# Optimization experiments

Hardware: AMD Instinct MI355X
Metric: run time of the kernel (lower is better)

Reference implementation:

```python
import jax, jax.numpy as jnp
import numpy as np

B, T, C, H, N = 4, 4096, 1024, 16, 64
D_DECAY, D_AAA, D_MV, D_GATE = 64, 64, 32, 160
EPS_GN = 1e-5 * 8 ** 2  # GroupNorm eps = 1e-5 * head_size_divisor**2


def _k(i):
    return jax.random.fold_in(jax.random.key(0), i)


def setup_inputs():
    p = {}
    p["x"] = jax.random.normal(_k(1), (B, T, C), jnp.float32)
    p["v_first"] = jax.random.normal(_k(2), (B, T, C), jnp.float32)
    for i, name in enumerate(["x_r", "x_w", "x_k", "x_v", "x_a", "x_g"]):
        p[name] = jax.random.uniform(_k(10 + i), (1, 1, C), jnp.float32)
    p["w0"] = jnp.linspace(-7.0, -2.0, C, dtype=jnp.float32).reshape(1, 1, C) + 0.5
    p["w1"] = jax.random.normal(_k(20), (C, D_DECAY), jnp.float32) * 0.02
    p["w2"] = jax.random.normal(_k(21), (D_DECAY, C), jnp.float32) * 0.02
    p["a0"] = jax.random.normal(_k(22), (1, 1, C), jnp.float32) * 0.02
    p["a1"] = jax.random.normal(_k(23), (C, D_AAA), jnp.float32) * 0.02
    p["a2"] = jax.random.normal(_k(24), (D_AAA, C), jnp.float32) * 0.02
    p["v0"] = jnp.ones((1, 1, C), jnp.float32)
    p["v1"] = jax.random.normal(_k(25), (C, D_MV), jnp.float32) * 0.02
    p["v2"] = jax.random.normal(_k(26), (D_MV, C), jnp.float32) * 0.02
    p["g1"] = jax.random.normal(_k(27), (C, D_GATE), jnp.float32) * 0.02
    p["g2"] = jax.random.normal(_k(28), (D_GATE, C), jnp.float32) * 0.02
    p["k_k"] = jnp.full((1, 1, C), 0.85, jnp.float32)
    p["k_a"] = jnp.ones((1, 1, C), jnp.float32)
    p["r_k"] = jax.random.normal(_k(29), (H, N), jnp.float32) * 0.02
    s = 0.5 / C ** 0.5
    p["Wr"] = jax.random.uniform(_k(30), (C, C), jnp.float32, -s, s)
    p["Wk"] = jax.random.uniform(_k(31), (C, C), jnp.float32, -0.1 * s, 0.1 * s)
    p["Wv"] = jax.random.uniform(_k(32), (C, C), jnp.float32, -s, s)
    p["Wo"] = jax.random.uniform(_k(33), (C, C), jnp.float32, -s, s)
    p["ln_w"] = jnp.ones((C,), jnp.float32)
    p["ln_b"] = jnp.zeros((C,), jnp.float32)
    p["alpha"] = jnp.array(0.5, jnp.float32)
    return p


def _wkv_scan(ins, reverse):
    # ins: tuple of time-major (T,B,H,N) arrays: r, decay, k, v, a, b
    def step(S, inp):
        r_t, d_t, k_t, v_t, a_t, b_t = inp
        sa = jnp.einsum('bhij,bhj->bhi', S, a_t)  # in-context removal term
        S = (S * d_t[:, :, None, :]
             + sa[..., None] * b_t[:, :, None, :]
             + v_t[..., None] * k_t[:, :, None, :])
        return S, jnp.einsum('bhij,bhj->bhi', S, r_t)
    S0 = jnp.zeros((B, H, N, N), jnp.float32)
    return jax.lax.scan(step, S0, ins, reverse=reverse)[1]


def reference(x, v_first, x_r, x_w, x_k, x_v, x_a, x_g, w0, w1, w2, a0, a1, a2,
              v0, v1, v2, g1, g2, k_k, k_a, r_k, Wr, Wk, Wv, Wo, ln_w, ln_b, alpha):
    xx = jnp.pad(x, ((0, 0), (1, 0), (0, 0)))[:, :T, :] - x  # token shift
    xr = x + xx * x_r
    xw = x + xx * x_w
    xk = x + xx * x_k
    xv = x + xx * x_v
    xa = x + xx * x_a
    xg = x + xx * x_g
    r = xr @ Wr.T
    w = -jax.nn.softplus(-(w0 + jnp.tanh(xw @ w1) @ w2)) - 0.5
    k = xk @ Wk.T
    v = xv @ Wv.T
    v = v + (v_first - v) * jax.nn.sigmoid(v0 + (xv @ v1) @ v2)  # layer_id != 0
    a = jax.nn.sigmoid(a0 + (xa @ a1) @ a2)
    g = jax.nn.sigmoid(xg @ g1) @ g2
    kk = (k * k_k).reshape(B, T, H, N)
    kk = kk / jnp.maximum(jnp.linalg.norm(kk, axis=-1, keepdims=True), 1e-12)
    k = k * (1.0 + (a - 1.0) * k_a)
    rh = r.reshape(B, T, H, N)
    kh = k.reshape(B, T, H, N)
    vh = v.reshape(B, T, H, N)
    dec = jnp.exp(-jnp.exp(w.reshape(B, T, H, N)))  # per-channel decay
    ah = -kk
    bh = kk * a.reshape(B, T, H, N)
    tm = lambda z: jnp.transpose(z, (1, 0, 2, 3))  # -> (T,B,H,N)
    ins = (tm(rh), tm(dec), tm(kh), tm(vh), tm(ah), tm(bh))
    y_f = _wkv_scan(ins, reverse=False)
    y_b = _wkv_scan(ins, reverse=True)
    y = alpha * y_f + (1.0 - alpha) * y_b  # bidirectional blend (alpha)
    y = jnp.transpose(y, (1, 0, 2, 3))  # (B,T,H,N)
    mu = y.mean(-1, keepdims=True)
    var = y.var(-1, keepdims=True)
    y = (y - mu) / jnp.sqrt(var + EPS_GN)  # GroupNorm(H groups)
    y = y * ln_w.reshape(1, 1, H, N) + ln_b.reshape(1, 1, H, N)
    y = y + (rh * kh * r_k).sum(-1, keepdims=True) * vh
    out = (y.reshape(B, T, C) * g) @ Wo.T
    return (out, v_first)
```

## Files before the change

### kernel.cpp

```cpp
#include <hip/hip_runtime.h>
#include <hip/hip_bf16.h>
#include <math.h>

#define BB 4
#define TT 4096
#define CC 1024
#define HH 16
#define NN 64
#define BT (BB*TT)
#define EPS_GN 6.4e-4f
#define TMAX (TT-1)
#define LCH 64
#define CB 8
#define NB 8
#define STR 68

typedef __attribute__((ext_vector_type(8))) short bf16x8;
typedef __attribute__((ext_vector_type(4))) float f32x4;

__device__ __forceinline__ float sigmoidf_(float x) {
    return 1.0f / (1.0f + expf(-x));
}

__device__ __forceinline__ float waveReduceSum(float v) {
    #pragma unroll
    for (int off = 32; off > 0; off >>= 1)
        v += __shfl_xor(v, off, 64);
    return v;
}

__device__ __forceinline__ unsigned short f2bf(float f) {
    unsigned u = __float_as_uint(f);
    u += 0x7FFFu + ((u >> 16) & 1u);
    return (unsigned short)(u >> 16);
}
__device__ __forceinline__ float bf2f(unsigned short h) {
    return __uint_as_float(((unsigned)h) << 16);
}

__device__ __forceinline__ void gll16(const unsigned short* g, unsigned short* l) {
    __builtin_amdgcn_global_load_lds(
        (__attribute__((address_space(1))) void*)(g),
        (__attribute__((address_space(3))) void*)(l), 16, 0, 0);
}

template<int SA0,int SA1,int SB0,int SB1>
__device__ __forceinline__ void gemm64(const float* __restrict__ A,
                                       const float* __restrict__ B,
                                       float acc[4][4], int tr, int tc) {
    #pragma unroll 2
    for (int kx = 0; kx < 64; kx += 4) {
        float a_[4][4];
        if (SA0 == 1) {
            #pragma unroll
            for (int kk = 0; kk < 4; kk++) {
                float4 t = *(const float4*)&A[tr + (kx + kk) * SA1];
                a_[0][kk] = t.x; a_[1][kk] = t.y; a_[2][kk] = t.z; a_[3][kk] = t.w;
            }
        } else {
            #pragma unroll
            for (int r = 0; r < 4; r++) {
                float4 t = *(const float4*)&A[(tr + r) * SA0 + kx];
                a_[r][0] = t.x; a_[r][1] = t.y; a_[r][2] = t.z; a_[r][3] = t.w;
            }
        }
        float b_[4][4];
        if (SB0 == 1) {
            #pragma unroll
            for (int kk = 0; kk < 4; kk++) {
                float4 t = *(const float4*)&B[tc + (kx + kk) * SB1];
                b_[0][kk] = t.x; b_[1][kk] = t.y; b_[2][kk] = t.z; b_[3][kk] = t.w;
            }
        } else {
            #pragma unroll
            for (int cq = 0; cq < 4; cq++) {
                float4 t = *(const float4*)&B[(tc + cq) * SB0 + kx];
                b_[cq][0] = t.x; b_[cq][1] = t.y; b_[cq][2] = t.z; b_[cq][3] = t.w;
            }
        }
        #pragma unroll
        for (int r = 0; r < 4; r++)
            #pragma unroll
            for (int cq = 0; cq < 4; cq++)
                #pragma unroll
                for (int kk = 0; kk < 4; kk++)
                    acc[r][cq] = fmaf(a_[r][kk], b_[cq][kk], acc[r][cq]);
    }
}

template<bool DOMIX>
__global__ __launch_bounds__(256) void conv_split(
    const float* __restrict__ X, const float* __restrict__ mix,
    unsigned short* __restrict__ Hi, unsigned short* __restrict__ Lo,
    int ngroups)
{
    int g = blockIdx.x * 256 + threadIdx.x;
    if (g >= ngroups) return;
    int m = g >> 7;
    int k = (g & 127) * 8;
    const float* px = X + (size_t)m * CC + k;
    float a[8];
    {
        float4 x0 = *(const float4*)px;
        float4 x1 = *(const float4*)(px + 4);
        a[0]=x0.x; a[1]=x0.y; a[2]=x0.z; a[3]=x0.w;
        a[4]=x1.x; a[5]=x1.y; a[6]=x1.z; a[7]=x1.w;
    }
    if (DOMIX) {
        float4 p0, p1;
        if ((m & (TT - 1)) == 0) {
            p0 = make_float4(0.f,0.f,0.f,0.f); p1 = p0;
        } else {
            p0 = *(const float4*)(px - CC);
            p1 = *(const float4*)(px - CC + 4);
        }
        float4 m0 = *(const float4*)(mix + k);
        float4 m1 = *(const float4*)(mix + k + 4);
        float pv[8] = {p0.x,p0.y,p0.z,p0.w,p1.x,p1.y,p1.z,p1.w};
        float mv[8] = {m0.x,m0.y,m0.z,m0.w,m1.x,m1.y,m1.z,m1.w};
        #pragma unroll
        for (int j = 0; j < 8; j++) a[j] += (pv[j] - a[j]) * mv[j];
    }
    unsigned short hi[8], lo[8];
    #pragma unroll
    for (int j = 0; j < 8; j++) {
        hi[j] = f2bf(a[j]);
        lo[j] = f2bf(a[j] - bf2f(hi[j]));
    }
    uint4 H, L;
    H.x = (unsigned)hi[0] | ((unsigned)hi[1] << 16);
    H.y = (unsigned)hi[2] | ((unsigned)hi[3] << 16);
    H.z = (unsigned)hi[4] | ((unsigned)hi[5] << 16);
    H.w = (unsigned)hi[6] | ((unsigned)hi[7] << 16);
    L.x = (unsigned)lo[0] | ((unsigned)lo[1] << 16);
    L.y = (unsigned)lo[2] | ((unsigned)lo[3] << 16);
    L.z = (unsigned)lo[4] | ((unsigned)lo[5] << 16);
    L.w = (unsigned)lo[6] | ((unsigned)lo[7] << 16);
    *(uint4*)(Hi + (size_t)g * 8) = H;
    *(uint4*)(Lo + (size_t)g * 8) = L;
}

__global__ __launch_bounds__(256) void conv_w2(
    const float* __restrict__ W, int K, int Kp,
    unsigned short* __restrict__ Hi, unsigned short* __restrict__ Lo)
{
    int idx = blockIdx.x * 256 + threadIdx.x;
    int nk8 = Kp >> 3;
    if (idx >= CC * nk8) return;
    int n = idx / nk8, k0 = (idx - n * nk8) * 8;
    unsigned short h8[8], l8[8];
    #pragma unroll
    for (int j = 0; j < 8; j++) {
        int k = k0 + j;
        float v = (k < K) ? W[(size_t)k * CC + n] : 0.f;
        h8[j] = f2bf(v);
        l8[j] = f2bf(v - bf2f(h8[j]));
    }
    uint4 H, L;
    H.x = (unsigned)h8[0] | ((unsigned)h8[1] << 16);
    H.y = (unsigned)h8[2] | ((unsigned)h8[3] << 16);
    H.z = (unsigned)h8[4] | ((unsigned)h8[5] << 16);
    H.w = (unsigned)h8[6] | ((unsigned)h8[7] << 16);
    L.x = (unsigned)l8[0] | ((unsigned)l8[1] << 16);
    L.y = (unsigned)l8[2] | ((unsigned)l8[3] << 16);
    L.z = (unsigned)l8[4] | ((unsigned)l8[5] << 16);
    L.w = (unsigned)l8[6] | ((unsigned)l8[7] << 16);
    *(uint4*)(Hi + (size_t)n * Kp + k0) = H;
    *(uint4*)(Lo + (size_t)n * Kp + k0) = L;
}

__global__ __launch_bounds__(256, 2) void gemm_split_bf16(
    const unsigned short* __restrict__ Ah, const unsigned short* __restrict__ Al,
    const unsigned short* __restrict__ Bh, const unsigned short* __restrict__ Bl,
    float* __restrict__ Out)
{
    __shared__ __align__(16) unsigned short lds[4][128 * 64];
    const int tid = threadIdx.x;
    const int lane = tid & 63;
    const int wave = tid >> 6;
    const int wm = (wave >> 1) * 64, wn = (wave & 1) * 64;
    const int wg = blockIdx.x;
    const int xcd = wg & 7;
    const int j = wg >> 3;
    const int m0 = ((j >> 3) * 8 + xcd) * 128;
    const int n0 = (j & 7) * 128;

    f32x4 acc[4][4];
    #pragma unroll
    for (int i = 0; i < 4; i++)
        #pragma unroll
        for (int jj = 0; jj < 4; jj++)
            acc[i][jj] = (f32x4){0.f, 0.f, 0.f, 0.f};

    for (int k0 = 0; k0 < CC; k0 += 64) {
        #pragma unroll
        for (int p = 0; p < 4; p++) {
            const unsigned short* sbase = (p == 0) ? Ah : (p == 1) ? Al
                                        : (p == 2) ? Bh : Bl;
            const int rbase = (p < 2) ? m0 : n0;
            #pragma unroll
            for (int i = 0; i < 4; i++) {
                int slot = i * 256 + wave * 64 + lane;
                int row = slot >> 3, gsl = slot & 7;
                const unsigned short* src = sbase
                    + (size_t)(rbase + row) * CC + k0 + ((gsl ^ (row & 7)) * 8);
                gll16(src, &lds[p][(size_t)(i * 256 + wave * 64) * 8]);
            }
        }
        __syncthreads();

        #pragma unroll
        for (int ks = 0; ks < 2; ks++) {
            bf16x8 bhf[4], blf[4];
            #pragma unroll
            for (int nt = 0; nt < 4; nt++) {
                int col = wn + nt * 16 + (lane & 15);
                int gk = ks * 4 + (lane >> 4);
                int el = col * 64 + ((gk ^ (col & 7)) * 8);
                bhf[nt] = *(const bf16x8*)&lds[2][el];
                blf[nt] = *(const bf16x8*)&lds[3][el];
            }
            #pragma unroll
            for (int mt = 0; mt < 4; mt++) {
                int row = wm + mt * 16 + (lane & 15);
                int gk = ks * 4 + (lane >> 4);
                int el = row * 64 + ((gk ^ (row & 7)) * 8);
                bf16x8 ahf = *(const bf16x8*)&lds[0][el];
                bf16x8 alf = *(const bf16x8*)&lds[1][el];
                #pragma unroll
                for (int nt = 0; nt < 4; nt++) {
                    acc[mt][nt] = __builtin_amdgcn_mfma_f32_16x16x32_bf16(
                        ahf, bhf[nt], acc[mt][nt], 0, 0, 0);
                    acc[mt][nt] = __builtin_amdgcn_mfma_f32_16x16x32_bf16(
                        alf, bhf[nt], acc[mt][nt], 0, 0, 0);
                    acc[mt][nt] = __builtin_amdgcn_mfma_f32_16x16x32_bf16(
                        ahf, blf[nt], acc[mt][nt], 0, 0, 0);
                }
            }
        }
        __syncthreads();
    }
    float* cf = (float*)&lds[0][0];
    #pragma unroll
    for (int pass = 0; pass < 2; ++pass) {
        __syncthreads();
        if ((wave >> 1) == pass) {
            #pragma unroll
            for (int mt = 0; mt < 4; mt++)
                #pragma unroll
                for (int nt = 0; nt < 4; nt++)
                    #pragma unroll
                    for (int r = 0; r < 4; r++) {
                        int row = mt * 16 + (lane >> 4) * 4 + r;
                        int col = wn + nt * 16 + (lane & 15);
                        cf[row * 132 + col] = acc[mt][nt][r];
                    }
        }
        __syncthreads();
        #pragma unroll
        for (int i = 0; i < 8; i++) {
            int g = tid + 256 * i;
            int row = g >> 5, c4 = (g & 31) * 4;
            float4 v = *(float4*)&cf[row * 132 + c4];
            *(float4*)&Out[(size_t)(m0 + pass * 64 + row) * CC + n0 + c4] = v;
        }
    }
}

__global__ __launch_bounds__(256) void lora1_all(
    const float* __restrict__ X,
    const float* __restrict__ w1, const float* __restrict__ a1,
    const float* __restrict__ v1, const float* __restrict__ g1,
    const float* __restrict__ xw, const float* __restrict__ xa,
    const float* __restrict__ xv, const float* __restrict__ xg,
    unsigned short* __restrict__ awh, unsigned short* __restrict__ awl,
    unsigned short* __restrict__ aah, unsigned short* __restrict__ aal,
    unsigned short* __restrict__ avh, unsigned short* __restrict__ avl,
    unsigned short* __restrict__ agh, unsigned short* __restrict__ agl)
{
    const int y = blockIdx.y;
    const float* W; const float* mix; unsigned short *Hi, *Lo;
    int Ncols, n0, epi, Kp;
    if (y == 0)      { W=w1; mix=xw; Hi=awh; Lo=awl; Ncols=64;  n0=0;          epi=1; Kp=64;  }
    else if (y == 1) { W=a1; mix=xa; Hi=aah; Lo=aal; Ncols=64;  n0=0;          epi=0; Kp=64;  }
    else if (y == 2) { W=v1; mix=xv; Hi=avh; Lo=avl; Ncols=32;  n0=0;          epi=0; Kp=64;  }
    else             { W=g1; mix=xg; Hi=agh; Lo=agl; Ncols=160; n0=(y-3)*64;   epi=2; Kp=192; }

    __shared__ float As[8][128];
    __shared__ float Bs[8][64];
    const int tid = threadIdx.x;
    const int m0 = blockIdx.x * 128;
    const int sr  = tid >> 1;
    const int skq = (tid & 1) * 4;
    const int bkr = tid >> 4;
    const int bnq = (tid & 15) * 4;
    const int tm = (tid >> 3) * 4;
    const int tn = (tid & 7) * 8;

    float acc[4][8];
    #pragma unroll
    for (int i = 0; i < 4; i++)
        #pragma unroll
        for (int j = 0; j < 8; j++) acc[i][j] = 0.f;

    auto ldAm = [&](int gm, int gk) -> float4 {
        const float* px = X + (size_t)gm * CC + gk;
        float4 xvv = *(const float4*)px;
        float4 pv;
        if ((gm & (TT - 1)) == 0) pv = make_float4(0.f, 0.f, 0.f, 0.f);
        else pv = *(const float4*)(px - CC);
        float4 mv = *(const float4*)(mix + gk);
        xvv.x += (pv.x - xvv.x) * mv.x;
        xvv.y += (pv.y - xvv.y) * mv.y;
        xvv.z += (pv.z - xvv.z) * mv.z;
        xvv.w += (pv.w - xvv.w) * mv.w;
        return xvv;
    };

    float4 aR, bR = make_float4(0.f, 0.f, 0.f, 0.f);
    aR = ldAm(m0 + sr, skq);
    if (tid < 128) {
        int gn = n0 + bnq;
        bR = (gn < Ncols) ? *(const float4*)(W + (size_t)bkr * Ncols + gn)
                          : make_float4(0.f, 0.f, 0.f, 0.f);
    }

    for (int k0 = 0; k0 < CC; k0 += 8) {
        __syncthreads();
        As[skq + 0][sr] = aR.x;
        As[skq + 1][sr] = aR.y;
        As[skq + 2][sr] = aR.z;
        As[skq + 3][sr] = aR.w;
        if (tid < 128) *(float4*)&Bs[bkr][bnq] = bR;
        __syncthreads();

        if (k0 + 8 < CC) {
            aR = ldAm(m0 + sr, k0 + 8 + skq);
            if (tid < 128) {
                int gn = n0 + bnq;
                bR = (gn < Ncols) ? *(const float4*)(W + (size_t)(k0 + 8 + bkr) * Ncols + gn)
                                  : make_float4(0.f, 0.f, 0.f, 0.f);
            }
        }

        #pragma unroll
        for (int kk = 0; kk < 8; ++kk) {
            float av[4], bv[8];
            *(float4*)&av[0] = *(const float4*)&As[kk][tm];
            *(float4*)&bv[0] = *(const float4*)&Bs[kk][tn];
            *(float4*)&bv[4] = *(const float4*)&Bs[kk][tn + 4];
            #pragma unroll
            for (int i = 0; i < 4; i++)
                #pragma unroll
                for (int j = 0; j < 8; j++)
                    acc[i][j] = fmaf(av[i], bv[j], acc[i][j]);
        }
    }

    #pragma unroll
    for (int i = 0; i < 4; i++) {
        int gm = m0 + tm + i;
        int gn = n0 + tn;
        if (gn < Kp) {
            unsigned short h8[8], l8[8];
            #pragma unroll
            for (int j = 0; j < 8; j++) {
                float v = 0.f;
                if (gn + j < Ncols) {
                    v = acc[i][j];
                    if (epi == 1) v = tanhf(v);
                    else if (epi == 2) v = sigmoidf_(v);
                }
                h8[j] = f2bf(v);
                l8[j] = f2bf(v - bf2f(h8[j]));
            }
            uint4 H, L;
            H.x = (unsigned)h8[0] | ((unsigned)h8[1] << 16);
            H.y = (unsigned)h8[2] | ((unsigned)h8[3] << 16);
            H.z = (unsigned)h8[4] | ((unsigned)h8[5] << 16);
            H.w = (unsigned)h8[6] | ((unsigned)h8[7] << 16);
            L.x = (unsigned)l8[0] | ((unsigned)l8[1] << 16);
            L.y = (unsigned)l8[2] | ((unsigned)l8[3] << 16);
            L.z = (unsigned)l8[4] | ((unsigned)l8[5] << 16);
            L.w = (unsigned)l8[6] | ((unsigned)l8[7] << 16);
            *(uint4*)(Hi + (size_t)gm * Kp + gn) = H;
            *(uint4*)(Lo + (size_t)gm * Kp + gn) = L;
        }
    }
}

__global__ __launch_bounds__(256, 2) void lora2_mfma(
    const unsigned short* __restrict__ awh, const unsigned short* __restrict__ awl,
    const unsigned short* __restrict__ aah, const unsigned short* __restrict__ aal,
    const unsigned short* __restrict__ avh, const unsigned short* __restrict__ avl,
    const unsigned short* __restrict__ agh, const unsigned short* __restrict__ agl,
    const unsigned short* __restrict__ w2h, const unsigned short* __restrict__ w2l,
    const unsigned short* __restrict__ a2h, const unsigned short* __restrict__ a2l,
    const unsigned short* __restrict__ v2h, const unsigned short* __restrict__ v2l,
    const unsigned short* __restrict__ g2h, const unsigned short* __restrict__ g2l,
    const float* __restrict__ w0, const float* __restrict__ a0v,
    const float* __restrict__ v0v, const float* __restrict__ v_first,
    float* __restrict__ decb, float* __restrict__ ab,
    float* __restrict__ vbuf, float* __restrict__ gb)
{
    __shared__ __align__(16) unsigned short lds[4][128 * 64];
    const int z = blockIdx.z;
    const unsigned short *Ah, *Al, *Bh, *Bl; int Kp;
    if (z == 0)      { Ah = awh; Al = awl; Bh = w2h; Bl = w2l; Kp = 64;  }
    else if (z == 1) { Ah = aah; Al = aal; Bh = a2h; Bl = a2l; Kp = 64;  }
    else if (z == 2) { Ah = avh; Al = avl; Bh = v2h; Bl = v2l; Kp = 64;  }
    else             { Ah = agh; Al = agl; Bh = g2h; Bl = g2l; Kp = 192; }

    const int tid = threadIdx.x, lane = tid & 63, wave = tid >> 6;
    const int wm = (wave >> 1) * 64, wn = (wave & 1) * 64;
    const int m0 = blockIdx.x * 128, n0 = blockIdx.y * 128;

    f32x4 acc[4][4];
    #pragma unroll
    for (int i = 0; i < 4; i++)
        #pragma unroll
        for (int jj = 0; jj < 4; jj++)
            acc[i][jj] = (f32x4){0.f, 0.f, 0.f, 0.f};

    for (int k0 = 0; k0 < Kp; k0 += 64) {
        #pragma unroll
        for (int p = 0; p < 4; p++) {
            const unsigned short* sbase = (p == 0) ? Ah : (p == 1) ? Al
                                        : (p == 2) ? Bh : Bl;
            const int rbase = (p < 2) ? m0 : n0;
            #pragma unroll
            for (int i = 0; i < 4; i++) {
                int slot = i * 256 + wave * 64 + lane;
                int row = slot >> 3, gsl = slot & 7;
                const unsigned short* src = sbase
                    + (size_t)(rbase + row) * Kp + k0 + ((gsl ^ (row & 7)) * 8);
                gll16(src, &lds[p][(size_t)(i * 256 + wave * 64) * 8]);
            }
        }
        __syncthreads();

        #pragma unroll
        for (int ks = 0; ks < 2; ks++) {
            bf16x8 bhf[4], blf[4];
            #pragma unroll
            for (int nt = 0; nt < 4; nt++) {
                int col = wn + nt * 16 + (lane & 15);
                int gk = ks * 4 + (lane >> 4);
                int el = col * 64 + ((gk ^ (col & 7)) * 8);
                bhf[nt] = *(const bf16x8*)&lds[2][el];
                blf[nt] = *(const bf16x8*)&lds[3][el];
            }
            #pragma unroll
            for (int mt = 0; mt < 4; mt++) {
                int row = wm + mt * 16 + (lane & 15);
                int gk = ks * 4 + (lane >> 4);
                int el = row * 64 + ((gk ^ (row & 7)) * 8);
                bf16x8 ahf = *(const bf16x8*)&lds[0][el];
                bf16x8 alf = *(const bf16x8*)&lds[1][el];
                #pragma unroll
                for (int nt = 0; nt < 4; nt++) {
                    acc[mt][nt] = __builtin_amdgcn_mfma_f32_16x16x32_bf16(
                        ahf, bhf[nt], acc[mt][nt], 0, 0, 0);
                    acc[mt][nt] = __builtin_amdgcn_mfma_f32_16x16x32_bf16(
                        alf, bhf[nt], acc[mt][nt], 0, 0, 0);
                    acc[mt][nt] = __builtin_amdgcn_mfma_f32_16x16x32_bf16(
                        ahf, blf[nt], acc[mt][nt], 0, 0, 0);
                }
            }
        }
        __syncthreads();
    }
    float* cf = (float*)&lds[0][0];
    #pragma unroll
    for (int pass = 0; pass < 2; ++pass) {
        __syncthreads();
        if ((wave >> 1) == pass) {
            #pragma unroll
            for (int mt = 0; mt < 4; mt++)
                #pragma unroll
                for (int nt = 0; nt < 4; nt++)
                    #pragma unroll
                    for (int r = 0; r < 4; r++) {
                        int row = mt * 16 + (lane >> 4) * 4 + r;
                        int col = wn + nt * 16 + (lane & 15);
                        cf[row * 132 + col] = acc[mt][nt][r];
                    }
        }
        __syncthreads();
        #pragma unroll
        for (int i = 0; i < 8; i++) {
            int g = tid + 256 * i;
            int row = g >> 5, c4 = (g & 31) * 4;
            float4 v = *(float4*)&cf[row * 132 + c4];
            int gm = m0 + pass * 64 + row;
            int c = n0 + c4;
            size_t off = (size_t)gm * CC + c;
            if (z == 0) {
                float4 w0q = *(const float4*)(w0 + c);
                float4 o;
                o.x = expf(-expf(-log1pf(expf(-(w0q.x + v.x))) - 0.5f));
                o.y = expf(-expf(-log1pf(expf(-(w0q.y + v.y))) - 0.5f));
                o.z = expf(-expf(-log1pf(expf(-(w0q.z + v.z))) - 0.5f));
                o.w = expf(-expf(-log1pf(expf(-(w0q.w + v.w))) - 0.5f));
                *(float4*)&decb[off] = o;
            } else if (z == 1) {
                float4 a0q = *(const float4*)(a0v + c);
                float4 o;
                o.x = sigmoidf_(a0q.x + v.x);
                o.y = sigmoidf_(a0q.y + v.y);
                o.z = sigmoidf_(a0q.z + v.z);
                o.w = sigmoidf_(a0q.w + v.w);
                *(float4*)&ab[off] = o;
            } else if (z == 2) {
                float4 v0q = *(const float4*)(v0v + c);
                float4 vr = *(const float4*)&vbuf[off];
                float4 vf = *(const float4*)&v_first[off];
                float4 o;
                o.x = vr.x + (vf.x - vr.x) * sigmoidf_(v0q.x + v.x);
                o.y = vr.y + (vf.y - vr.y) * sigmoidf_(v0q.y + v.y);
                o.z = vr.z + (vf.z - vr.z) * sigmoidf_(v0q.z + v.z);
                o.w = vr.w + (vf.w - vr.w) * sigmoidf_(v0q.w + v.w);
                *(float4*)&vbuf[off] = o;
            } else {
                *(float4*)&gb[off] = v;
            }
        }
    }
}

__global__ __launch_bounds__(256) void wkvA(
    const float* __restrict__ kb, const float* __restrict__ ab,
    const float* __restrict__ vb, const float* __restrict__ decb,
    const float* __restrict__ k_k, const float* __restrict__ k_a,
    float* __restrict__ Gb, float* __restrict__ Ub,
    float* __restrict__ Bpb, float* __restrict__ Kpb,
    float* __restrict__ wcb, int cb)
{
    __shared__ __align__(16) float sAp[64 * STR];
    __shared__ __align__(16) float sBp[64 * STR];
    __shared__ __align__(16) float sKp[64 * STR];
    __shared__ __align__(16) float sT [64 * STR];
    __shared__ float sSeg[4][64];
    const int inst = blockIdx.x;
    const int bhd = inst >> 3, lc = inst & 7;
    const int dir = bhd & 1, bh = bhd >> 1, b = bh >> 4, h = bh & 15;
    const int c64 = (cb * CB + lc) * LCH;
    const int tid = threadIdx.x;
    const int lane = tid & 63, seg = tid >> 6;
    const int ch = h * 64 + lane;
    const size_t gbase = (size_t)inst * 4096;

    float loc[16];
    {
        float run = 1.f;
        #pragma unroll
        for (int i = 0; i < 16; i++) {
            int p = seg * 16 + i;
            int t = dir ? (TMAX - (c64 + p)) : (c64 + p);
            float d = decb[((size_t)(b * TT + t)) * CC + ch];
            run *= d; loc[i] = run;
        }
        sSeg[seg][lane] = run;
    }
    __syncthreads();
    float pre = 1.f;
    for (int s2 = 0; s2 < seg; ++s2) pre *= sSeg[s2][lane];
    {
        const float kkl = k_k[ch], kal = k_a[ch];
        #pragma unroll
        for (int i = 0; i < 16; i++) {
            int p = seg * 16 + i;
            int t = dir ? (TMAX - (c64 + p)) : (c64 + p);
            size_t ra = ((size_t)(b * TT + t)) * CC + ch;
            float kraw = kb[ra], asig = ab[ra];
            float kkv = kraw * kkl;
            float s2 = waveReduceSum(kkv * kkv);
            float kkn = kkv / fmaxf(sqrtf(s2), 1e-12f);
            float wc = loc[i] * pre;
            float wx = (i == 0) ? pre : loc[i - 1] * pre;
            float apv = -kkn * wx;
            float bpv = kkn * asig / wc;
            float kpv = kraw * (1.f + (asig - 1.f) * kal) / wc;
            sAp[lane * STR + p] = apv;
            sBp[lane * STR + p] = bpv;
            sKp[lane * STR + p] = kpv;
            Bpb[gbase + p * 64 + lane] = bpv;
            Kpb[gbase + p * 64 + lane] = kpv;
            wcb[gbase + p * 64 + lane] = wc;
        }
    }
    __syncthreads();

    const int tr = (tid >> 4) * 4, tc = (tid & 15) * 4;
    {
        float acc[4][4] = {};
        gemm64<1, STR, 1, STR>(sAp, sKp, acc, tr, tc);
        #pragma unroll
        for (int r = 0; r < 4; r++)
            #pragma unroll
            for (int cq = 0; cq < 4; cq++)
                sT[(tr + r) * STR + tc + cq] = (tc + cq < tr + r) ? acc[r][cq] : 0.f;
    }
    __syncthreads();
    {
        float accY[4][4] = {};
        const float* vbase = vb + ((size_t)(b * TT + (dir ? (TMAX - c64) : c64))) * CC
                           + h * 64 + tc;
        const ptrdiff_t vstep = dir ? -(ptrdiff_t)CC : (ptrdiff_t)CC;
        #pragma unroll 2
        for (int j4 = 0; j4 < 64; j4 += 4) {
            float a_[4][4];
            #pragma unroll
            for (int r = 0; r < 4; r++) {
                float4 t4 = *(const float4*)&sT[(tr + r) * STR + j4];
                a_[r][0] = t4.x; a_[r][1] = t4.y; a_[r][2] = t4.z; a_[r][3] = t4.w;
            }
            float4 vq[4];
            #pragma unroll
            for (int kk = 0; kk < 4; kk++)
                vq[kk] = *(const float4*)(vbase + (ptrdiff_t)(j4 + kk) * vstep);
            #pragma unroll
            for (int r = 0; r < 4; r++) {
                accY[r][0] = fmaf(a_[r][0], vq[0].x, fmaf(a_[r][1], vq[1].x,
                             fmaf(a_[r][2], vq[2].x, fmaf(a_[r][3], vq[3].x, accY[r][0]))));
                accY[r][1] = fmaf(a_[r][0], vq[0].y, fmaf(a_[r][1], vq[1].y,
                             fmaf(a_[r][2], vq[2].y, fmaf(a_[r][3], vq[3].y, accY[r][1]))));
                accY[r][2] = fmaf(a_[r][0], vq[0].z, fmaf(a_[r][1], vq[1].z,
                             fmaf(a_[r][2], vq[2].z, fmaf(a_[r][3], vq[3].z, accY[r][2]))));
                accY[r][3] = fmaf(a_[r][0], vq[0].w, fmaf(a_[r][1], vq[1].w,
                             fmaf(a_[r][2], vq[2].w, fmaf(a_[r][3], vq[3].w, accY[r][3]))));
            }
        }
        #pragma unroll
        for (int r = 0; r < 4; r++)
            #pragma unroll
            for (int cq = 0; cq < 4; cq++)
                sKp[(tr + r) * STR + tc + cq] = accY[r][cq];
    }
    __syncthreads();
    {
        float acc[4][4] = {};
        gemm64<1, STR, 1, STR>(sAp, sBp, acc, tr, tc);
        #pragma unroll
        for (int r = 0; r < 4; r++)
            #pragma unroll
            for (int cq = 0; cq < 4; cq++)
                sT[(tr + r) * STR + tc + cq] = (tc + cq < tr + r) ? acc[r][cq] : 0.f;
    }
    __syncthreads();
    if (tid < 64) {
        for (int r = 0; r < 64; ++r) {
            float acc = 0.f;
            for (int s = 0; s < r; ++s)
                acc = fmaf(sT[r * STR + s], sBp[s * STR + tid], acc);
            sBp[r * STR + tid] = (r == tid) ? 1.f : acc;
        }
    }
    __syncthreads();
    {
        float accG[4][4] = {};
        gemm64<STR, 1, STR, 1>(sBp, sAp, accG, tr, tc);
        float accU[4][4] = {};
        gemm64<STR, 1, 1, STR>(sBp, sKp, accU, tr, tc);
        #pragma unroll
        for (int r = 0; r < 4; r++) {
            *(float4*)&Gb[gbase + (tr + r) * 64 + tc] =
                make_float4(accG[r][0], accG[r][1], accG[r][2], accG[r][3]);
            *(float4*)&Ub[gbase + (tr + r) * 64 + tc] =
                make_float4(accU[r][0], accU[r][1], accU[r][2], accU[r][3]);
        }
    }
}

__global__ __launch_bounds__(256) void wkvB(
    const float* __restrict__ vb,
    const float* __restrict__ Gb, float* __restrict__ Ub,
    const float* __restrict__ Bpb, const float* __restrict__ Kpb,
    const float* __restrict__ wcb, float* __restrict__ S0b,
    float* __restrict__ Scur, int cb)
{
    __shared__ __align__(16) float sS[64 * STR];
    __shared__ __align__(16) float sG[64 * STR];
    __shared__ __align__(16) float sU[64 * STR];
    __shared__ __align__(16) float sB[64 * STR];
    __shared__ __align__(16) float sK[64 * STR];
    __shared__ __align__(16) float sV[64 * STR];
    const int bhd = blockIdx.x;
    const int dir = bhd & 1, bh = bhd >> 1, b = bh >> 4, h = bh & 15;
    const int tid = threadIdx.x;
    const int tr = (tid >> 4) * 4, tc = (tid & 15) * 4;

    for (int i = tid; i < 4096; i += 256)
        sS[(i >> 6) * STR + (i & 63)] = Scur[(size_t)bhd * 4096 + i];
    __syncthreads();

    for (int lc = 0; lc < CB; ++lc) {
        const int inst = bhd * CB + lc;
        const size_t gbase = (size_t)inst * 4096;
        const int c64 = (cb * CB + lc) * LCH;
        for (int i = tid; i < 4096; i += 256) {
            int rr = i >> 6, jj = i & 63;
            sG[rr * STR + jj] = Gb[gbase + i];
            sB[rr * STR + jj] = Bpb[gbase + i];
            sK[rr * STR + jj] = Kpb[gbase + i];
            int t = dir ? (TMAX - (c64 + rr)) : (c64 + rr);
            sV[rr * STR + jj] = vb[((size_t)(b * TT + t)) * CC + h * 64 + jj];
            S0b[gbase + i] = sS[rr * STR + jj];
        }
        __syncthreads();
        {
            float acc[4][4];
            #pragma unroll
            for (int r = 0; r < 4; r++) {
                float4 u0 = *(const float4*)&Ub[gbase + (tr + r) * 64 + tc];
                acc[r][0] = u0.x; acc[r][1] = u0.y; acc[r][2] = u0.z; acc[r][3] = u0.w;
            }
            gemm64<STR, 1, STR, 1>(sG, sS, acc, tr, tc);
            #pragma unroll
            for (int r = 0; r < 4; r++) {
                #pragma unroll
                for (int cq = 0; cq < 4; cq++) sU[(tr + r) * STR + tc + cq] = acc[r][cq];
                *(float4*)&Ub[gbase + (tr + r) * 64 + tc] =
                    make_float4(acc[r][0], acc[r][1], acc[r][2], acc[r][3]);
            }
        }
        __syncthreads();
        {
            float acc[4][4] = {};
            gemm64<1, STR, 1, STR>(sU, sB, acc, tr, tc);
            gemm64<1, STR, 1, STR>(sV, sK, acc, tr, tc);
            float w63[4];
            #pragma unroll
            for (int cq = 0; cq < 4; cq++) w63[cq] = wcb[gbase + 63 * 64 + tc + cq];
            #pragma unroll
            for (int r = 0; r < 4; r++)
                #pragma unroll
                for (int cq = 0; cq < 4; cq++) {
                    float sv = sS[(tr + r) * STR + tc + cq];
                    acc[r][cq] = (sv + acc[r][cq]) * w63[cq];
                }
            #pragma unroll
            for (int r = 0; r < 4; r++)
                #pragma unroll
                for (int cq = 0; cq < 4; cq++)
                    sS[(tr + r) * STR + tc + cq] = acc[r][cq];
        }
        __syncthreads();
    }
    for (int i = tid; i < 4096; i += 256)
        Scur[(size_t)bhd * 4096 + i] = sS[(i >> 6) * STR + (i & 63)];
}

__global__ __launch_bounds__(256) void wkvC(
    const float* __restrict__ rb, const float* __restrict__ vb,
    const float* __restrict__ Bpb, const float* __restrict__ Kpb,
    const float* __restrict__ Ub, const float* __restrict__ S0b,
    const float* __restrict__ wcb, const float* __restrict__ alpha_p,
    float* __restrict__ yb, int cb)
{
    __shared__ __align__(16) float sR[64 * STR];
    __shared__ __align__(16) float sO[64 * STR];
    __shared__ __align__(16) float sT2[64 * STR];
    const int inst = blockIdx.x;
    const int bhd = inst >> 3, lc = inst & 7;
    const int dir = bhd & 1, bh = bhd >> 1, b = bh >> 4, h = bh & 15;
    const int c64 = (cb * CB + lc) * LCH;
    const int tid = threadIdx.x, lane = tid & 63, seg = tid >> 6;
    const size_t gbase = (size_t)inst * 4096;
    const float alpha = alpha_p[0];
    const float wscale = dir ? (1.f - alpha) : alpha;
    const bool first = (cb < NB / 2);

    #pragma unroll
    for (int i = 0; i < 16; i++) {
        int p = seg * 16 + i;
        int t = dir ? (TMAX - (c64 + p)) : (c64 + p);
        size_t ra = ((size_t)(b * TT + t)) * CC + h * 64 + lane;
        float wc = wcb[gbase + p * 64 + lane];
        sR[lane * STR + p] = rb[ra] * wc;
        sO[lane * STR + p] = Bpb[gbase + p * 64 + lane];
    }
    __syncthreads();
    const int tr = (tid >> 4) * 4, tc = (tid & 15) * 4;
    float accO[4][4] = {};
    {
        float acc[4][4] = {};
        gemm64<1, STR, 1, STR>(sR, sO, acc, tr, tc);
        #pragma unroll
        for (int r = 0; r < 4; r++)
            #pragma unroll
            for (int cq = 0; cq < 4; cq++)
                sT2[(tr + r) * STR + tc + cq] = (tc + cq <= tr + r) ? acc[r][cq] : 0.f;
    }
    __syncthreads();
    for (int i = tid; i < 4096; i += 256)
        sO[(i >> 6) * STR + (i & 63)] = Ub[gbase + i];
    __syncthreads();
    gemm64<STR, 1, 1, STR>(sT2, sO, accO, tr, tc);
    __syncthreads();
    #pragma unroll
    for (int i = 0; i < 16; i++) {
        int p = seg * 16 + i;
        sO[lane * STR + p] = Kpb[gbase + p * 64 + lane];
    }
    __syncthreads();
    {
        float acc[4][4] = {};
        gemm64<1, STR, 1, STR>(sR, sO, acc, tr, tc);
        #pragma unroll
        for (int r = 0; r < 4; r++)
            #pragma unroll
            for (int cq = 0; cq < 4; cq++)
                sT2[(tr + r) * STR + tc + cq] = (tc + cq <= tr + r) ? acc[r][cq] : 0.f;
    }
    __syncthreads();
    #pragma unroll
    for (int i = 0; i < 16; i++) {
        int p = seg * 16 + i;
        int t = dir ? (TMAX - (c64 + p)) : (c64 + p);
        sO[p * STR + lane] = vb[((size_t)(b * TT + t)) * CC + h * 64 + lane];
    }
    __syncthreads();
    gemm64<STR, 1, 1, STR>(sT2, sO, accO, tr, tc);
    __syncthreads();
    for (int i = tid; i < 4096; i += 256)
        sO[(i >> 6) * STR + (i & 63)] = S0b[gbase + i];
    __syncthreads();
    gemm64<1, STR, STR, 1>(sR, sO, accO, tr, tc);
    #pragma unroll
    for (int r = 0; r < 4; r++) {
        int p = tr + r;
        int t = dir ? (TMAX - (c64 + p)) : (c64 + p);
        float* yp = &yb[((size_t)(b * TT + t)) * CC + h * 64 + tc];
        float4 o;
        if (first) {
            o.x = wscale * accO[r][0];
            o.y = wscale * accO[r][1];
            o.z = wscale * accO[r][2];
            o.w = wscale * accO[r][3];
        } else {
            float4 old = *(float4*)yp;
            o.x = old.x + wscale * accO[r][0];
            o.y = old.y + wscale * accO[r][1];
            o.z = old.z + wscale * accO[r][2];
            o.w = old.w + wscale * accO[r][3];
        }
        *(float4*)yp = o;
    }
}

__global__ __launch_bounds__(256) void post_kernel(
    const float* __restrict__ yb, const float* __restrict__ rbv,
    const float* __restrict__ kbv, const float* __restrict__ abv,
    const float* __restrict__ vbv, const float* __restrict__ gbv,
    const float* __restrict__ kaw, const float* __restrict__ r_k,
    const float* __restrict__ ln_w, const float* __restrict__ ln_b,
    unsigned short* __restrict__ zh, unsigned short* __restrict__ zl)
{
    const int t = blockIdx.x;
    const int tid = threadIdx.x;
    const size_t base = (size_t)t * CC;
    #pragma unroll
    for (int j = 0; j < 4; j++) {
        int c = tid + 256 * j;
        float y = yb[base + c];
        float s1 = waveReduceSum(y);
        float s2 = waveReduceSum(y * y);
        float mu = s1 * (1.0f / 64.0f);
        float var = s2 * (1.0f / 64.0f) - mu * mu;
        float yn = (y - mu) * rsqrtf(var + EPS_GN);
        yn = yn * ln_w[c] + ln_b[c];
        float rv = rbv[base + c];
        float kf = kbv[base + c] * (1.0f + (abv[base + c] - 1.0f) * kaw[c]);
        float vv = vbv[base + c];
        float dot = waveReduceSum(rv * kf * r_k[c]);
        yn += dot * vv;
        float z = yn * gbv[base + c];
        unsigned short h = f2bf(z);
        zh[base + c] = h;
        zl[base + c] = f2bf(z - bf2f(h));
    }
}

extern "C" void kernel_launch(void* const* d_in, const int* in_sizes, int n_in,
                              void* d_out, int out_size, void* d_ws, size_t ws_size,
                              hipStream_t stream)
{
    (void)in_sizes; (void)n_in; (void)out_size; (void)ws_size;
    const float* x      = (const float*)d_in[0];
    const float* vfirst = (const float*)d_in[1];
    const float* x_r    = (const float*)d_in[2];
    const float* x_w    = (const float*)d_in[3];
    const float* x_k    = (const float*)d_in[4];
    const float* x_v    = (const float*)d_in[5];
    const float* x_a    = (const float*)d_in[6];
    const float* x_g    = (const float*)d_in[7];
    const float* w0     = (const float*)d_in[8];
    const float* w1     = (const float*)d_in[9];
    const float* w2     = (const float*)d_in[10];
    const float* a0     = (const float*)d_in[11];
    const float* a1     = (const float*)d_in[12];
    const float* a2     = (const float*)d_in[13];
    const float* v0     = (const float*)d_in[14];
    const float* v1     = (const float*)d_in[15];
    const float* v2     = (const float*)d_in[16];
    const float* g1     = (const float*)d_in[17];
    const float* g2     = (const float*)d_in[18];
    const float* k_k    = (const float*)d_in[19];
    const float* k_a    = (const float*)d_in[20];
    const float* r_k    = (const float*)d_in[21];
    const float* Wr     = (const float*)d_in[22];
    const float* Wk     = (const float*)d_in[23];
    const float* Wv     = (const float*)d_in[24];
    const float* Wo     = (const float*)d_in[25];
    const float* ln_w   = (const float*)d_in[26];
    const float* ln_b   = (const float*)d_in[27];
    const float* alpha  = (const float*)d_in[28];

    const size_t SZ = (size_t)BT * CC;
    const size_t CHB = (size_t)1024 * 4096;
    float* ws   = (float*)d_ws;
    float* rb   = ws + 0 * SZ;
    float* kb   = ws + 1 * SZ;
    float* vb   = ws + 2 * SZ;
    float* decb = ws + 3 * SZ;
    float* ab   = ws + 4 * SZ;
    float* actf = ws + 5 * SZ;
    unsigned short* awh = (unsigned short*)actf;
    unsigned short* awl = awh + (size_t)BT * 64;
    unsigned short* aah = awl + (size_t)BT * 64;
    unsigned short* aal = aah + (size_t)BT * 64;
    unsigned short* avh = aal + (size_t)BT * 64;
    unsigned short* avl = avh + (size_t)BT * 64;
    unsigned short* agh = avl + (size_t)BT * 64;
    unsigned short* agl = agh + (size_t)BT * 192;
    float* Gb   = actf + (size_t)BT * 384;
    float* Ub   = Gb + CHB;
    float* Bpb  = Ub + CHB;
    float* Kpb  = Bpb + CHB;
    float* S0b  = Kpb + CHB;
    float* wcb  = S0b + CHB;
    float* Scur = wcb + CHB;
    unsigned short* Whb = (unsigned short*)(Scur + (size_t)128 * 4096);
    unsigned short* Wlb = Whb + (size_t)CC * CC;
    unsigned short* w2th = Wlb + (size_t)CC * CC;
    unsigned short* w2tl = w2th + (size_t)CC * 64;
    unsigned short* a2th = w2tl + (size_t)CC * 64;
    unsigned short* a2tl = a2th + (size_t)CC * 64;
    unsigned short* v2th = a2tl + (size_t)CC * 64;
    unsigned short* v2tl = v2th + (size_t)CC * 64;
    unsigned short* g2th = v2tl + (size_t)CC * 64;
    unsigned short* g2tl = g2th + (size_t)CC * 192;
    float* outp = (float*)d_out;
    float* gb   = outp;
    float* yb   = outp + SZ;
    unsigned short* Ahp = (unsigned short*)(outp + SZ);
    unsigned short* Alp = Ahp + SZ;
    unsigned short* zAh = (unsigned short*)decb;
    unsigned short* zAl = zAh + SZ;

    dim3 blk(256);
    const int NG_A = BT * (CC / 8);
    const int NG_W = CC * (CC / 8);
    dim3 gridA(NG_A / 256), gridW(NG_W / 256);
    dim3 gridG(1024);

    conv_split<false><<<gridW, blk, 0, stream>>>(Wr, nullptr, Whb, Wlb, NG_W);
    conv_split<true ><<<gridA, blk, 0, stream>>>(x, x_r, Ahp, Alp, NG_A);
    gemm_split_bf16<<<gridG, blk, 0, stream>>>(Ahp, Alp, Whb, Wlb, rb);
    conv_split<false><<<gridW, blk, 0, stream>>>(Wk, nullptr, Whb, Wlb, NG_W);
    conv_split<true ><<<gridA, blk, 0, stream>>>(x, x_k, Ahp, Alp, NG_A);
    gemm_split_bf16<<<gridG, blk, 0, stream>>>(Ahp, Alp, Whb, Wlb, kb);
    conv_split<false><<<gridW, blk, 0, stream>>>(Wv, nullptr, Whb, Wlb, NG_W);
    conv_split<true ><<<gridA, blk, 0, stream>>>(x, x_v, Ahp, Alp, NG_A);
    gemm_split_bf16<<<gridG, blk, 0, stream>>>(Ahp, Alp, Whb, Wlb, vb);

    conv_w2<<<dim3(32), blk, 0, stream>>>(w2, 64, 64, w2th, w2tl);
    conv_w2<<<dim3(32), blk, 0, stream>>>(a2, 64, 64, a2th, a2tl);
    conv_w2<<<dim3(32), blk, 0, stream>>>(v2, 32, 64, v2th, v2tl);
    conv_w2<<<dim3(96), blk, 0, stream>>>(g2, 160, 192, g2th, g2tl);

    lora1_all<<<dim3(BT / 128, 6), blk, 0, stream>>>(x, w1, a1, v1, g1,
        x_w, x_a, x_v, x_g, awh, awl, aah, aal, avh, avl, agh, agl);
    lora2_mfma<<<dim3(BT / 128, CC / 128, 4), blk, 0, stream>>>(
        awh, awl, aah, aal, avh, avl, agh, agl,
        w2th, w2tl, a2th, a2tl, v2th, v2tl, g2th, g2tl,
        w0, a0, v0, vfirst, decb, ab, vb, gb);

    hipMemsetAsync(Scur, 0, (size_t)128 * 4096 * sizeof(float), stream);
    for (int cb = 0; cb < NB; ++cb) {
        wkvA<<<dim3(1024), blk, 0, stream>>>(kb, ab, vb, decb, k_k, k_a,
                                             Gb, Ub, Bpb, Kpb, wcb, cb);
        wkvB<<<dim3(128), blk, 0, stream>>>(vb, Gb, Ub, Bpb, Kpb, wcb, S0b, Scur, cb);
        wkvC<<<dim3(1024), blk, 0, stream>>>(rb, vb, Bpb, Kpb, Ub, S0b, wcb,
                                             alpha, yb, cb);
    }

    post_kernel<<<dim3(BT), blk, 0, stream>>>(yb, rb, kb, ab, vb, gb, k_a, r_k,
                                              ln_w, ln_b, zAh, zAl);
    conv_split<false><<<gridW, blk, 0, stream>>>(Wo, nullptr, Whb, Wlb, NG_W);
    hipMemcpyAsync(outp + SZ, vfirst, SZ * sizeof(float),
                   hipMemcpyDeviceToDevice, stream);
    gemm_split_bf16<<<gridG, blk, 0, stream>>>(zAh, zAl, Whb, Wlb, outp);
}
```

Measured before the change: 3.212 ms.

## Fuse token-shift bf16 split for r/k/v inputs and retile lora2 to 128x64

A new kernel reads x and its shifted row once and writes the bf16 hi/lo splits for the r, k and v mixes together. This replaces three separate conversion passes that each re-read x. The lora2 MFMA kernel moves from 128x128 to 128x64 tiles with less LDS and a simpler single-pass epilogue, so more blocks fit per CU. In exchange, the r/k/v split buffers now live in the output and decay scratch regions, which must not be overwritten before the GEMMs consume them.

Result: faster. 3.111 ms (-3.1%).

```diff
diff --git a/kernel.cpp b/kernel.cpp
--- a/kernel.cpp
+++ b/kernel.cpp
@@ -138,6 +138,63 @@
     L.w = (unsigned)lo[6] | ((unsigned)lo[7] << 16);
     *(uint4*)(Hi + (size_t)g * 8) = H;
     *(uint4*)(Lo + (size_t)g * 8) = L;
+}
+
+__global__ __launch_bounds__(256) void conv_split_x3(
+    const float* __restrict__ X,
+    const float* __restrict__ mr, const float* __restrict__ mk,
+    const float* __restrict__ mv,
+    unsigned short* __restrict__ rH, unsigned short* __restrict__ rL,
+    unsigned short* __restrict__ kH, unsigned short* __restrict__ kL,
+    unsigned short* __restrict__ vH, unsigned short* __restrict__ vL)
+{
+    int g = blockIdx.x * 256 + threadIdx.x;
+    int m = g >> 7;
+    int k = (g & 127) * 8;
+    const float* px = X + (size_t)m * CC + k;
+    float xv8[8], pv[8];
+    {
+        float4 x0 = *(const float4*)px;
+        float4 x1 = *(const float4*)(px + 4);
+        xv8[0]=x0.x; xv8[1]=x0.y; xv8[2]=x0.z; xv8[3]=x0.w;
+        xv8[4]=x1.x; xv8[5]=x1.y; xv8[6]=x1.z; xv8[7]=x1.w;
+    }
+    if ((m & (TT - 1)) == 0) {
+        #pragma unroll
+        for (int j = 0; j < 8; j++) pv[j] = 0.f;
+    } else {
+        float4 p0 = *(const float4*)(px - CC);
+        float4 p1 = *(const float4*)(px - CC + 4);
+        pv[0]=p0.x; pv[1]=p0.y; pv[2]=p0.z; pv[3]=p0.w;
+        pv[4]=p1.x; pv[5]=p1.y; pv[6]=p1.z; pv[7]=p1.w;
+    }
+    const float* mixes[3] = {mr, mk, mv};
+    unsigned short* His[3] = {rH, kH, vH};
+    unsigned short* Los[3] = {rL, kL, vL};
+    #pragma unroll
+    for (int s = 0; s < 3; s++) {
+        float4 m0 = *(const float4*)(mixes[s] + k);
+        float4 m1 = *(const float4*)(mixes[s] + k + 4);
+        float mv8[8] = {m0.x,m0.y,m0.z,m0.w,m1.x,m1.y,m1.z,m1.w};
+        unsigned short hi[8], lo[8];
+        #pragma unroll
+        for (int j = 0; j < 8; j++) {
+            float a = xv8[j] + (pv[j] - xv8[j]) * mv8[j];
+            hi[j] = f2bf(a);
+            lo[j] = f2bf(a - bf2f(hi[j]));
+        }
+        uint4 H, L;
+        H.x = (unsigned)hi[0] | ((unsigned)hi[1] << 16);
+        H.y = (unsigned)hi[2] | ((unsigned)hi[3] << 16);
+        H.z = (unsigned)hi[4] | ((unsigned)hi[5] << 16);
+        H.w = (unsigned)hi[6] | ((unsigned)hi[7] << 16);
+        L.x = (unsigned)lo[0] | ((unsigned)lo[1] << 16);
+        L.y = (unsigned)lo[2] | ((unsigned)lo[3] << 16);
+        L.z = (unsigned)lo[4] | ((unsigned)lo[5] << 16);
+        L.w = (unsigned)lo[6] | ((unsigned)lo[7] << 16);
+        *(uint4*)(His[s] + (size_t)g * 8) = H;
+        *(uint4*)(Los[s] + (size_t)g * 8) = L;
+    }
 }
 
 __global__ __launch_bounds__(256) void conv_w2(
@@ -389,7 +446,7 @@
     }
 }
 
-__global__ __launch_bounds__(256, 2) void lora2_mfma(
+__global__ __launch_bounds__(256, 3) void lora2_mfma(
     const unsigned short* __restrict__ awh, const unsigned short* __restrict__ awl,
     const unsigned short* __restrict__ aah, const unsigned short* __restrict__ aal,
     const unsigned short* __restrict__ avh, const unsigned short* __restrict__ avl,
@@ -403,7 +460,7 @@
     float* __restrict__ decb, float* __restrict__ ab,
     float* __restrict__ vbuf, float* __restrict__ gb)
 {
-    __shared__ __align__(16) unsigned short lds[4][128 * 64];
+    __shared__ __align__(16) unsigned short lds[24576];
     const int z = blockIdx.z;
     const unsigned short *Ah, *Al, *Bh, *Bl; int Kp;
     if (z == 0)      { Ah = awh; Al = awl; Bh = w2h; Bl = w2l; Kp = 64;  }
@@ -412,53 +469,63 @@
     else             { Ah = agh; Al = agl; Bh = g2h; Bl = g2l; Kp = 192; }
 
     const int tid = threadIdx.x, lane = tid & 63, wave = tid >> 6;
-    const int wm = (wave >> 1) * 64, wn = (wave & 1) * 64;
-    const int m0 = blockIdx.x * 128, n0 = blockIdx.y * 128;
-
-    f32x4 acc[4][4];
+    const int wm = (wave >> 1) * 64, wn = (wave & 1) * 32;
+    const int m0 = blockIdx.x * 128, n0 = blockIdx.y * 64;
+
+    f32x4 acc[4][2];
     #pragma unroll
     for (int i = 0; i < 4; i++)
         #pragma unroll
-        for (int jj = 0; jj < 4; jj++)
+        for (int jj = 0; jj < 2; jj++)
             acc[i][jj] = (f32x4){0.f, 0.f, 0.f, 0.f};
 
     for (int k0 = 0; k0 < Kp; k0 += 64) {
         #pragma unroll
-        for (int p = 0; p < 4; p++) {
-            const unsigned short* sbase = (p == 0) ? Ah : (p == 1) ? Al
-                                        : (p == 2) ? Bh : Bl;
-            const int rbase = (p < 2) ? m0 : n0;
+        for (int p = 0; p < 2; p++) {
+            const unsigned short* sbase = (p == 0) ? Ah : Al;
             #pragma unroll
             for (int i = 0; i < 4; i++) {
                 int slot = i * 256 + wave * 64 + lane;
                 int row = slot >> 3, gsl = slot & 7;
                 const unsigned short* src = sbase
-                    + (size_t)(rbase + row) * Kp + k0 + ((gsl ^ (row & 7)) * 8);
-                gll16(src, &lds[p][(size_t)(i * 256 + wave * 64) * 8]);
+                    + (size_t)(m0 + row) * Kp + k0 + ((gsl ^ (row & 7)) * 8);
+                gll16(src, &lds[(size_t)(p * 8192) + (size_t)(i * 256 + wave * 64) * 8]);
+            }
+        }
+        #pragma unroll
+        for (int p = 0; p < 2; p++) {
+            const unsigned short* sbase = (p == 0) ? Bh : Bl;
+            #pragma unroll
+            for (int i = 0; i < 2; i++) {
+                int slot = i * 256 + wave * 64 + lane;
+                int row = slot >> 3, gsl = slot & 7;
+                const unsigned short* src = sbase
+                    + (size_t)(n0 + row) * Kp + k0 + ((gsl ^ (row & 7)) * 8);
+                gll16(src, &lds[(size_t)(16384 + p * 4096) + (size_t)(i * 256 + wave * 64) * 8]);
             }
         }
         __syncthreads();
 
         #pragma unroll
         for (int ks = 0; ks < 2; ks++) {
-            bf16x8 bhf[4], blf[4];
-            #pragma unroll
-            for (int nt = 0; nt < 4; nt++) {
+            bf16x8 bhf[2], blf[2];
+            #pragma unroll
+            for (int nt = 0; nt < 2; nt++) {
                 int col = wn + nt * 16 + (lane & 15);
                 int gk = ks * 4 + (lane >> 4);
                 int el = col * 64 + ((gk ^ (col & 7)) * 8);
-                bhf[nt] = *(const bf16x8*)&lds[2][el];
-                blf[nt] = *(const bf16x8*)&lds[3][el];
+                bhf[nt] = *(const bf16x8*)&lds[16384 + el];
+                blf[nt] = *(const bf16x8*)&lds[20480 + el];
             }
             #pragma unroll
             for (int mt = 0; mt < 4; mt++) {
                 int row = wm + mt * 16 + (lane & 15);
                 int gk = ks * 4 + (lane >> 4);
                 int el = row * 64 + ((gk ^ (row & 7)) * 8);
-                bf16x8 ahf = *(const bf16x8*)&lds[0][el];
-                bf16x8 alf = *(const bf16x8*)&lds[1][el];
+                bf16x8 ahf = *(const bf16x8*)&lds[el];
+                bf16x8 alf = *(const bf16x8*)&lds[8192 + el];
                 #pragma unroll
-                for (int nt = 0; nt < 4; nt++) {
+                for (int nt = 0; nt < 2; nt++) {
                     acc[mt][nt] = __builtin_amdgcn_mfma_f32_16x16x32_bf16(
                         ahf, bhf[nt], acc[mt][nt], 0, 0, 0);
                     acc[mt][nt] = __builtin_amdgcn_mfma_f32_16x16x32_bf16(
@@ -470,60 +537,54 @@
         }
         __syncthreads();
     }
-    float* cf = (float*)&lds[0][0];
-    #pragma unroll
-    for (int pass = 0; pass < 2; ++pass) {
-        __syncthreads();
-        if ((wave >> 1) == pass) {
-            #pragma unroll
-            for (int mt = 0; mt < 4; mt++)
-                #pragma unroll
-                for (int nt = 0; nt < 4; nt++)
-                    #pragma unroll
-                    for (int r = 0; r < 4; r++) {
-                        int row = mt * 16 + (lane >> 4) * 4 + r;
-                        int col = wn + nt * 16 + (lane & 15);
-                        cf[row * 132 + col] = acc[mt][nt][r];
-                    }
-        }
-        __syncthreads();
-        #pragma unroll
-        for (int i = 0; i < 8; i++) {
-            int g = tid + 256 * i;
-            int row = g >> 5, c4 = (g & 31) * 4;
-            float4 v = *(float4*)&cf[row * 132 + c4];
-            int gm = m0 + pass * 64 + row;
-            int c = n0 + c4;
-            size_t off = (size_t)gm * CC + c;
-            if (z == 0) {
-                float4 w0q = *(const float4*)(w0 + c);
-                float4 o;
-                o.x = expf(-expf(-log1pf(expf(-(w0q.x + v.x))) - 0.5f));
-                o.y = expf(-expf(-log1pf(expf(-(w0q.y + v.y))) - 0.5f));
-                o.z = expf(-expf(-log1pf(expf(-(w0q.z + v.z))) - 0.5f));
-                o.w = expf(-expf(-log1pf(expf(-(w0q.w + v.w))) - 0.5f));
-                *(float4*)&decb[off] = o;
-            } else if (z == 1) {
-                float4 a0q = *(const float4*)(a0v + c);
-                float4 o;
-                o.x = sigmoidf_(a0q.x + v.x);
-                o.y = sigmoidf_(a0q.y + v.y);
-                o.z = sigmoidf_(a0q.z + v.z);
-                o.w = sigmoidf_(a0q.w + v.w);
-                *(float4*)&ab[off] = o;
-            } else if (z == 2) {
-                float4 v0q = *(const float4*)(v0v + c);
-                float4 vr = *(const float4*)&vbuf[off];
-                float4 vf = *(const float4*)&v_first[off];
-                float4 o;
-                o.x = vr.x + (vf.x - vr.x) * sigmoidf_(v0q.x + v.x);
-                o.y = vr.y + (vf.y - vr.y) * sigmoidf_(v0q.y + v.y);
-                o.z = vr.z + (vf.z - vr.z) * sigmoidf_(v0q.z + v.z);
-                o.w = vr.w + (vf.w - vr.w) * sigmoidf_(v0q.w + v.w);
-                *(float4*)&vbuf[off] = o;
-            } else {
-                *(float4*)&gb[off] = v;
-            }
+    float* cf = (float*)&lds[0];
+    #pragma unroll
+    for (int mt = 0; mt < 4; mt++)
+        #pragma unroll
+        for (int nt = 0; nt < 2; nt++)
+            #pragma unroll
+            for (int r = 0; r < 4; r++) {
+                int row = wm + mt * 16 + (lane >> 4) * 4 + r;
+                int col = wn + nt * 16 + (lane & 15);
+                cf[row * 68 + col] = acc[mt][nt][r];
+            }
+    __syncthreads();
+    #pragma unroll
+    for (int i = 0; i < 8; i++) {
+        int idx = tid + 256 * i;
+        int row = idx >> 4, c4 = (idx & 15) * 4;
+        float4 v = *(float4*)&cf[row * 68 + c4];
+        int gm = m0 + row;
+        int c = n0 + c4;
+        size_t off = (size_t)gm * CC + c;
+        if (z == 0) {
+            float4 w0q = *(const float4*)(w0 + c);
+            float4 o;
+            o.x = expf(-expf(-log1pf(expf(-(w0q.x + v.x))) - 0.5f));
+            o.y = expf(-expf(-log1pf(expf(-(w0q.y + v.y))) - 0.5f));
+            o.z = expf(-expf(-log1pf(expf(-(w0q.z + v.z))) - 0.5f));
+            o.w = expf(-expf(-log1pf(expf(-(w0q.w + v.w))) - 0.5f));
+            *(float4*)&decb[off] = o;
+        } else if (z == 1) {
+            float4 a0q = *(const float4*)(a0v + c);
+            float4 o;
+            o.x = sigmoidf_(a0q.x + v.x);
+            o.y = sigmoidf_(a0q.y + v.y);
+            o.z = sigmoidf_(a0q.z + v.z);
+            o.w = sigmoidf_(a0q.w + v.w);
+            *(float4*)&ab[off] = o;
+        } else if (z == 2) {
+            float4 v0q = *(const float4*)(v0v + c);
+            float4 vr = *(const float4*)&vbuf[off];
+            float4 vf = *(const float4*)&v_first[off];
+            float4 o;
+            o.x = vr.x + (vf.x - vr.x) * sigmoidf_(v0q.x + v.x);
+            o.y = vr.y + (vf.y - vr.y) * sigmoidf_(v0q.y + v.y);
+            o.z = vr.z + (vf.z - vr.z) * sigmoidf_(v0q.z + v.z);
+            o.w = vr.w + (vf.w - vr.w) * sigmoidf_(v0q.w + v.w);
+            *(float4*)&vbuf[off] = o;
+        } else {
+            *(float4*)&gb[off] = v;
         }
     }
 }
@@ -952,10 +1013,14 @@
     unsigned short* g2th = v2tl + (size_t)CC * 64;
     unsigned short* g2tl = g2th + (size_t)CC * 192;
     float* outp = (float*)d_out;
+    unsigned short* xrh = (unsigned short*)outp;
+    unsigned short* xrl = xrh + SZ;
+    unsigned short* xkh = xrl + SZ;
+    unsigned short* xkl = xkh + SZ;
+    unsigned short* xvh = (unsigned short*)decb;
+    unsigned short* xvl = xvh + SZ;
     float* gb   = outp;
     float* yb   = outp + SZ;
-    unsigned short* Ahp = (unsigned short*)(outp + SZ);
-    unsigned short* Alp = Ahp + SZ;
     unsigned short* zAh = (unsigned short*)decb;
     unsigned short* zAl = zAh + SZ;
 
@@ -965,15 +1030,14 @@
     dim3 gridA(NG_A / 256), gridW(NG_W / 256);
     dim3 gridG(1024);
 
+    conv_split_x3<<<gridA, blk, 0, stream>>>(x, x_r, x_k, x_v,
+                                             xrh, xrl, xkh, xkl, xvh, xvl);
     conv_split<false><<<gridW, blk, 0, stream>>>(Wr, nullptr, Whb, Wlb, NG_W);
-    conv_split<true ><<<gridA, blk, 0, stream>>>(x, x_r, Ahp, Alp, NG_A);
-    gemm_split_bf16<<<gridG, blk, 0, stream>>>(Ahp, Alp, Whb, Wlb, rb);
+    gemm_split_bf16<<<gridG, blk, 0, stream>>>(xrh, xrl, Whb, Wlb, rb);
     conv_split<false><<<gridW, blk, 0, stream>>>(Wk, nullptr, Whb, Wlb, NG_W);
-    conv_split<true ><<<gridA, blk, 0, stream>>>(x, x_k, Ahp, Alp, NG_A);
-    gemm_split_bf16<<<gridG, blk, 0, stream>>>(Ahp, Alp, Whb, Wlb, kb);
+    gemm_split_bf16<<<gridG, blk, 0, stream>>>(xkh, xkl, Whb, Wlb, kb);
     conv_split<false><<<gridW, blk, 0, stream>>>(Wv, nullptr, Whb, Wlb, NG_W);
-    conv_split<true ><<<gridA, blk, 0, stream>>>(x, x_v, Ahp, Alp, NG_A);
-    gemm_split_bf16<<<gridG, blk, 0, stream>>>(Ahp, Alp, Whb, Wlb, vb);
+    gemm_split_bf16<<<gridG, blk, 0, stream>>>(xvh, xvl, Whb, Wlb, vb);
 
     conv_w2<<<dim3(32), blk, 0, stream>>>(w2, 64, 64, w2th, w2tl);
     conv_w2<<<dim3(32), blk, 0, stream>>>(a2, 64, 64, a2th, a2tl);
@@ -982,7 +1046,7 @@
 
     lora1_all<<<dim3(BT / 128, 6), blk, 0, stream>>>(x, w1, a1, v1, g1,
         x_w, x_a, x_v, x_g, awh, awl, aah, aal, avh, avl, agh, agl);
-    lora2_mfma<<<dim3(BT / 128, CC / 128, 4), blk, 0, stream>>>(
+    lora2_mfma<<<dim3(BT / 128, CC / 64, 4), blk, 0, stream>>>(
         awh, awl, aah, aal, avh, avl, agh, agl,
         w2th, w2tl, a2th, a2tl, v2th, v2tl, g2th, g2tl,
         w0, a0, v0, vfirst, decb, ab, vb, gb);
```
